# Optimization experiments

Hardware: AMD Instinct MI355X
Metric: run time of the kernel (lower is better)

The kernel has to match this reference:

```python
import jax, jax.numpy as jnp
import numpy as np
from jax import lax

EPS = 1e-8
ROOT_2 = 1.41421
STYLE_SIZE = 512
OUT_CH = 512
STYLE_SCALE = (2.0 / STYLE_SIZE) ** 0.5   # Weight_Scaling(style_size): equalized-LR sqrt(2/fan_in)
OUT_SCALE = (2.0 / (OUT_CH * 1 * 1)) ** 0.5  # Weight_Scaling(out_channels*1*1)


def setup_inputs() -> dict:
    key = jax.random.key(0)
    ks = jax.random.split(key, 10)
    B, Cin, Cout, H, S = 8, 512, 512, 32, 512
    return {
        "x": jax.random.normal(ks[0], (B, Cin, H, H), dtype=jnp.float32),
        "style_base": jax.random.normal(ks[1], (B, S), dtype=jnp.float32),
        "noise": jax.random.normal(ks[2], (B, 1, 2 * H, 2 * H), dtype=jnp.float32),
        "t": jax.random.normal(ks[3], (B, Cout, 2 * H, 2 * H), dtype=jnp.float32),
        # learned params
        "affine_w": jax.random.normal(ks[4], (Cin, S), dtype=jnp.float32) * (1.0 / np.sqrt(S)),
        "affine_b": jnp.zeros((Cin,), dtype=jnp.float32),
        "conv_w": jax.random.normal(ks[5], (Cout, Cin, 3, 3), dtype=jnp.float32),
        "conv_b": jnp.zeros((1, Cout, 1, 1), dtype=jnp.float32),
        "prelu_a": jnp.asarray(0.25, dtype=jnp.float32),
        "noise_scalar": jnp.zeros((1, Cout, 1, 1), dtype=jnp.float32) + 0.1,
        "out_w": jax.random.normal(ks[6], (3, Cout, 1, 1), dtype=jnp.float32) * (1.0 / np.sqrt(Cout)),
        "out_b": jnp.zeros((3,), dtype=jnp.float32),
    }


def reference(x, style_base, noise, t, affine_w, affine_b, conv_w, conv_b,
              prelu_a, noise_scalar, out_w, out_b):
    B, Cin, H, W = x.shape
    # style_std = affine(Weight_Scaling(style_base)) + 1  -> [B, Cin]
    style_std = (style_base * STYLE_SCALE) @ affine_w.T + affine_b + 1.0

    # bilinear x2 upsample (align_corners=False == half-pixel, matches jax.image.resize)
    x = jax.image.resize(x, (B, Cin, 2 * H, 2 * W), method="bilinear")

    # modulated conv with L2 demodulation, expressed as input-scale + conv + output-scale
    # per-sample weight w_b[o,i,k,l] = w[o,i,k,l]*s[b,i] / ||w*s||_b,o
    wsq = jnp.sum(conv_w ** 2, axis=(2, 3))                      # [O, I]
    demod = 1.0 / jnp.sqrt(jnp.einsum("oi,bi->bo", wsq, style_std ** 2) + EPS)  # [B, O]
    xm = x * style_std[:, :, None, None]
    y = lax.conv_general_dilated(xm, conv_w, (1, 1), "SAME",
                                 dimension_numbers=("NCHW", "OIHW", "NCHW"))
    y = y * demod[:, :, None, None] + conv_b + noise_scalar * noise
    # PReLU (single shared slope)
    y = jnp.where(y >= 0, y, prelu_a * y)

    # out branch: skip add, scale, toRGB 1x1 conv, clamp
    y = (y + t) / ROOT_2
    out = lax.conv_general_dilated(y * OUT_SCALE, out_w, (1, 1), "SAME",
                                   dimension_numbers=("NCHW", "OIHW", "NCHW"))
    out = jnp.clip(out + out_b[None, :, None, None], 0.0, 1.0)
    return (y, out)
```

## Files before the change

kernel.cpp:

```cpp
#include <hip/hip_runtime.h>


typedef short bf16x8 __attribute__((ext_vector_type(8)));
typedef short short8v __attribute__((ext_vector_type(8)));
typedef float f32x16 __attribute__((ext_vector_type(16)));

#define WS_STYLE 0
#define WS_DEMOD 16384
#define WS_WSQ   32768
#define WS_WPACK 1081344
#define WS_XM    5799936

__device__ __forceinline__ short f2bf(float f) {
  unsigned u = __float_as_uint(f);
  u += 0x7FFFu + ((u >> 16) & 1u);
  return (short)(u >> 16);
}

__device__ __forceinline__ void gld16(const short* g, char* l) {
  __builtin_amdgcn_global_load_lds((const __attribute__((address_space(1))) void*)g,
                                   (__attribute__((address_space(3))) void*)l,
                                   16, 0, 0);
}

__global__ void k_style(const float* __restrict__ sb, const float* __restrict__ aw,
                        const float* __restrict__ ab, float* __restrict__ style) {
  __shared__ float s_sb[512];
  int b = blockIdx.x;
  for (int i = threadIdx.x; i < 512; i += 256) s_sb[i] = sb[b * 512 + i] * 0.0625f;
  __syncthreads();
  for (int i = threadIdx.x; i < 512; i += 256) {
    const float4* wrow = (const float4*)(aw + (size_t)i * 512);
    float acc = 0.f;
    #pragma unroll 4
    for (int s4 = 0; s4 < 128; ++s4) {
      float4 w4 = wrow[s4];
      float4 sv = *(const float4*)(s_sb + s4 * 4);
      acc += w4.x * sv.x + w4.y * sv.y + w4.z * sv.z + w4.w * sv.w;
    }
    style[b * 512 + i] = acc + ab[i] + 1.0f;
  }
}

__global__ void k_wsq(const float* __restrict__ cw, float* __restrict__ wsq) {
  int idx = blockIdx.x * 256 + threadIdx.x;
  const float* p = cw + (size_t)idx * 9;
  float s = 0.f;
  #pragma unroll
  for (int j = 0; j < 9; ++j) s += p[j] * p[j];
  wsq[idx] = s;
}

__global__ void k_demod(const float* __restrict__ wsq, const float* __restrict__ style,
                        float* __restrict__ demod) {
  int wid = threadIdx.x >> 6, lane = threadIdx.x & 63;
  int idx = blockIdx.x * 4 + wid;
  int b = idx >> 9, o = idx & 511;
  const float* wr = wsq + (size_t)o * 512;
  const float* ss = style + b * 512;
  float sum = 0.f;
  #pragma unroll
  for (int k = 0; k < 8; ++k) {
    int i = k * 64 + lane;
    float s = ss[i];
    sum += wr[i] * s * s;
  }
  #pragma unroll
  for (int off = 32; off; off >>= 1) sum += __shfl_down(sum, off);
  if (lane == 0) demod[b * 512 + o] = rsqrtf(sum + 1e-8f);
}

__global__ void k_upsample(const float* __restrict__ x, const float* __restrict__ style,
                           short* __restrict__ xm) {
  int b = blockIdx.x / 66, hp = blockIdx.x % 66;
  short* xmp = xm + ((size_t)b * 66 + hp) * 66 * 512;
  if (hp == 0 || hp == 65) {
    short8v z = {0, 0, 0, 0, 0, 0, 0, 0};
    for (int u = threadIdx.x; u < 66 * 512 / 8; u += 256) ((short8v*)xmp)[u] = z;
    return;
  }
  int h = hp - 1;
  int j0 = (h >> 1) - 1 + (h & 1);
  float fj = (h & 1) ? 0.25f : 0.75f;
  int j0c = j0 < 0 ? 0 : j0;
  int j1c = j0 + 1 > 31 ? 31 : j0 + 1;
  __shared__ float xt[2][64][33];
  int ccc = threadIdx.x & 63;
  int wsub = threadIdx.x >> 6;
  for (int c0 = 0; c0 < 512; c0 += 64) {
    __syncthreads();
    #pragma unroll 4
    for (int k = 0; k < 16; ++k) {
      int idx = k * 256 + threadIdx.x;
      int ii = idx & 31, cc = (idx >> 5) & 63, jj = idx >> 11;
      xt[jj][cc][ii] = x[(((size_t)b * 512 + c0 + cc) * 32 + (jj ? j1c : j0c)) * 32 + ii];
    }
    __syncthreads();
    float sstyle = style[b * 512 + c0 + ccc];
    #pragma unroll 4
    for (int wk = 0; wk < 16; ++wk) {
      int w = wk * 4 + wsub;
      int i0 = (w >> 1) - 1 + (w & 1);
      float fi = (w & 1) ? 0.25f : 0.75f;
      int i0c = i0 < 0 ? 0 : i0;
      int i1c = i0 + 1 > 31 ? 31 : i0 + 1;
      float v0 = xt[0][ccc][i0c] * (1.f - fi) + xt[0][ccc][i1c] * fi;
      float v1 = xt[1][ccc][i0c] * (1.f - fi) + xt[1][ccc][i1c] * fi;
      float v = (v0 * (1.f - fj) + v1 * fj) * sstyle;
      xmp[(size_t)(w + 1) * 512 + c0 + ccc] = f2bf(v);
    }
    if (wsub == 0) {
      xmp[c0 + ccc] = 0;
      xmp[(size_t)65 * 512 + c0 + ccc] = 0;
    }
  }
}

__global__ void k_packw(const float* __restrict__ cw, short* __restrict__ wpk) {
  int unit = blockIdx.x * 256 + threadIdx.x;
  int s = unit >> 11;
  int rem = unit & 2047;
  int o = rem >> 2, kg = rem & 3;
  int tap = s >> 4, cc = s & 15;
  int i0 = cc * 32 + (kg << 3);
  const float* src = cw + ((size_t)o * 512 + i0) * 9 + tap;
  short8v v;
  #pragma unroll
  for (int j = 0; j < 8; ++j) v[j] = f2bf(src[j * 9]);
  *(short8v*)(wpk + (size_t)unit * 8) = v;
}

__global__ __launch_bounds__(256, 2) void k_conv(
    const short* __restrict__ xm, const short* __restrict__ wpk,
    const float* __restrict__ demod, const float* __restrict__ convb,
    const float* __restrict__ nscal, const float* __restrict__ noise,
    const float* __restrict__ t, const float* __restrict__ prelu_a,
    float* __restrict__ y) {
  __shared__ char XMs[2][16896];

  int tid = threadIdx.x;
  int bid = blockIdx.x;
  int nt = bid & 1, hpair = (bid >> 1) & 31, b = bid >> 6;
  int wid = tid >> 6, lane = tid & 63;
  int wo = wid & 1, wsrow = wid >> 1;
  int l31 = lane & 31, lg = lane >> 5;

  const short* xb = xm + ((size_t)b * 66 + hpair * 2) * 66 * 512;
  const short* wlp = wpk + (size_t)((nt * 256 + wo * 128 + l31) * 32 + lg * 8);

  #pragma unroll
  for (int k = 0; k < 4; ++k) {
    int u = k * 256 + tid;
    int r = u / 264, rem = u - r * 264;
    int wp = rem >> 2, spp = rem & 3;
    gld16(xb + (size_t)(r * 66 + wp) * 512 + ((spp ^ ((wp >> 1) & 3)) << 3), XMs[0] + u * 16);
  }
  if (tid < 32) {
    int u = 1024 + tid;
    int rem = u - 792;
    int wp = rem >> 2, spp = rem & 3;
    gld16(xb + (size_t)(3 * 66 + wp) * 512 + ((spp ^ ((wp >> 1) & 3)) << 3), XMs[0] + u * 16);
  }

  bf16x8 wc0 = *(const bf16x8*)(wlp + 0);
  bf16x8 wc1 = *(const bf16x8*)(wlp + 1024);
  bf16x8 wc2 = *(const bf16x8*)(wlp + 2048);
  bf16x8 wc3 = *(const bf16x8*)(wlp + 3072);
  bf16x8 wc4 = *(const bf16x8*)(wlp + 16);
  bf16x8 wc5 = *(const bf16x8*)(wlp + 1040);
  bf16x8 wc6 = *(const bf16x8*)(wlp + 2064);
  bf16x8 wc7 = *(const bf16x8*)(wlp + 3088);

  f32x16 zf = {0,0,0,0,0,0,0,0,0,0,0,0,0,0,0,0};
  f32x16 acc[4][2];
  #pragma unroll
  for (int i = 0; i < 4; ++i) { acc[i][0] = zf; acc[i][1] = zf; }

  asm volatile("s_waitcnt vmcnt(0) lgkmcnt(0)" ::: "memory");
  __builtin_amdgcn_s_barrier();
  __builtin_amdgcn_sched_barrier(0);

  #pragma unroll 1
  for (int cc = 0; cc < 16; ++cc) {
    const char* XMc = XMs[cc & 1];
    char* XMn = XMs[(cc & 1) ^ 1];
    #pragma unroll
    for (int tap = 0; tap < 9; ++tap) {
      const int kh = tap / 3, kw = tap % 3;

      bf16x8 wn0, wn1, wn2, wn3, wn4, wn5, wn6, wn7;
      {
        int ntap = (tap < 8) ? (tap + 1) : 0;
        int ncc  = (tap < 8) ? cc : (cc + 1 < 16 ? cc + 1 : 15);
        const short* wsrc = wlp + (size_t)(ntap * 16 + ncc) * 16384;
        wn0 = *(const bf16x8*)(wsrc + 0);
        wn1 = *(const bf16x8*)(wsrc + 1024);
        wn2 = *(const bf16x8*)(wsrc + 2048);
        wn3 = *(const bf16x8*)(wsrc + 3072);
        wn4 = *(const bf16x8*)(wsrc + 16);
        wn5 = *(const bf16x8*)(wsrc + 1040);
        wn6 = *(const bf16x8*)(wsrc + 2064);
        wn7 = *(const bf16x8*)(wsrc + 3088);
      }
      if (tap <= 5 && cc < 15 && tid < 176) {
        int u = tap * 176 + tid;
        int r = u / 264, rem = u - r * 264;
        int wp = rem >> 2, spp = rem & 3;
        gld16(xb + (size_t)(r * 66 + wp) * 512 + (cc + 1) * 32 + ((spp ^ ((wp >> 1) & 3)) << 3),
              XMn + u * 16);
      }

      int a = l31 + kw;
      int xo = ((wsrow + kh) * 66 + a) * 64 + ((lg ^ ((a >> 1) & 3)) << 4);
      bf16x8 xf00 = *(const bf16x8*)(XMc + xo);
      bf16x8 xf01 = *(const bf16x8*)(XMc + xo + 2048);
      bf16x8 xf10 = *(const bf16x8*)(XMc + (xo ^ 32));
      bf16x8 xf11 = *(const bf16x8*)(XMc + ((xo ^ 32) + 2048));

      __builtin_amdgcn_s_setprio(1);
      acc[0][0] = __builtin_amdgcn_mfma_f32_32x32x16_bf16(wc0, xf00, acc[0][0], 0, 0, 0);
      acc[0][1] = __builtin_amdgcn_mfma_f32_32x32x16_bf16(wc0, xf01, acc[0][1], 0, 0, 0);
      acc[1][0] = __builtin_amdgcn_mfma_f32_32x32x16_bf16(wc1, xf00, acc[1][0], 0, 0, 0);
      acc[1][1] = __builtin_amdgcn_mfma_f32_32x32x16_bf16(wc1, xf01, acc[1][1], 0, 0, 0);
      acc[2][0] = __builtin_amdgcn_mfma_f32_32x32x16_bf16(wc2, xf00, acc[2][0], 0, 0, 0);
      acc[2][1] = __builtin_amdgcn_mfma_f32_32x32x16_bf16(wc2, xf01, acc[2][1], 0, 0, 0);
      acc[3][0] = __builtin_amdgcn_mfma_f32_32x32x16_bf16(wc3, xf00, acc[3][0], 0, 0, 0);
      acc[3][1] = __builtin_amdgcn_mfma_f32_32x32x16_bf16(wc3, xf01, acc[3][1], 0, 0, 0);
      acc[0][0] = __builtin_amdgcn_mfma_f32_32x32x16_bf16(wc4, xf10, acc[0][0], 0, 0, 0);
      acc[0][1] = __builtin_amdgcn_mfma_f32_32x32x16_bf16(wc4, xf11, acc[0][1], 0, 0, 0);
      acc[1][0] = __builtin_amdgcn_mfma_f32_32x32x16_bf16(wc5, xf10, acc[1][0], 0, 0, 0);
      acc[1][1] = __builtin_amdgcn_mfma_f32_32x32x16_bf16(wc5, xf11, acc[1][1], 0, 0, 0);
      acc[2][0] = __builtin_amdgcn_mfma_f32_32x32x16_bf16(wc6, xf10, acc[2][0], 0, 0, 0);
      acc[2][1] = __builtin_amdgcn_mfma_f32_32x32x16_bf16(wc6, xf11, acc[2][1], 0, 0, 0);
      acc[3][0] = __builtin_amdgcn_mfma_f32_32x32x16_bf16(wc7, xf10, acc[3][0], 0, 0, 0);
      acc[3][1] = __builtin_amdgcn_mfma_f32_32x32x16_bf16(wc7, xf11, acc[3][1], 0, 0, 0);
      __builtin_amdgcn_s_setprio(0);

      wc0 = wn0; wc1 = wn1; wc2 = wn2; wc3 = wn3;
      wc4 = wn4; wc5 = wn5; wc6 = wn6; wc7 = wn7;

      if (tap == 8) {
        asm volatile("s_waitcnt vmcnt(0) lgkmcnt(0)" ::: "memory");
        __builtin_amdgcn_s_barrier();
        __builtin_amdgcn_sched_barrier(0);
      }
    }
  }

  float pa = prelu_a[0];
  const float inv_r2 = 1.0f / 1.41421f;
  int h = hpair * 2 + wsrow;
  float nz0 = noise[((size_t)b * 64 + h) * 64 + l31];
  float nz1 = noise[((size_t)b * 64 + h) * 64 + 32 + l31];
  #pragma unroll
  for (int cf = 0; cf < 4; ++cf) {
    #pragma unroll
    for (int reg = 0; reg < 16; ++reg) {
      int orow = (reg & 3) + 8 * (reg >> 2) + 4 * lg;
      int o = nt * 256 + wo * 128 + cf * 32 + orow;
      float dm = demod[b * 512 + o];
      float cb = convb[o];
      float ns = nscal[o];
      #pragma unroll
      for (int nf = 0; nf < 2; ++nf) {
        int w = nf * 32 + l31;
        float v = acc[cf][nf][reg];
        v = v * dm + cb + ns * (nf ? nz1 : nz0);
        v = (v >= 0.f) ? v : pa * v;
        size_t oi = (((size_t)b * 512 + o) * 64 + h) * 64 + w;
        v = (v + t[oi]) * inv_r2;
        y[oi] = v;
      }
    }
  }
}

__global__ void k_rgb(const float* __restrict__ y, const float* __restrict__ ow,
                      const float* __restrict__ ob, float* __restrict__ out) {
  int b = blockIdx.x >> 6, h = blockIdx.x & 63;
  int w = threadIdx.x & 63, g = threadIdx.x >> 6;
  const float* yb = y + (((size_t)b * 512) * 64 + h) * 64 + w;
  float s0 = 0.f, s1 = 0.f, s2 = 0.f;
  for (int o = g * 128; o < g * 128 + 128; ++o) {
    float v = yb[(size_t)o * 4096];
    s0 += v * ow[o];
    s1 += v * ow[512 + o];
    s2 += v * ow[1024 + o];
  }
  __shared__ float red[3][4][64];
  red[0][g][w] = s0; red[1][g][w] = s1; red[2][g][w] = s2;
  __syncthreads();
  if (threadIdx.x < 192) {
    int c = threadIdx.x >> 6, ww = threadIdx.x & 63;
    float s = red[c][0][ww] + red[c][1][ww] + red[c][2][ww] + red[c][3][ww];
    s = s * 0.0625f + ob[c];
    s = fminf(fmaxf(s, 0.f), 1.f);
    out[(((size_t)b * 3 + c) * 64 + h) * 64 + ww] = s;
  }
}

extern "C" void kernel_launch(void* const* d_in, const int* in_sizes, int n_in,
                              void* d_out, int out_size, void* d_ws, size_t ws_size,
                              hipStream_t stream) {
  const float* x     = (const float*)d_in[0];
  const float* sb    = (const float*)d_in[1];
  const float* noise = (const float*)d_in[2];
  const float* t     = (const float*)d_in[3];
  const float* aw    = (const float*)d_in[4];
  const float* ab    = (const float*)d_in[5];
  const float* cw    = (const float*)d_in[6];
  const float* cb    = (const float*)d_in[7];
  const float* pa    = (const float*)d_in[8];
  const float* ns    = (const float*)d_in[9];
  const float* ow    = (const float*)d_in[10];
  const float* ob    = (const float*)d_in[11];
  char* ws = (char*)d_ws;
  float* style = (float*)(ws + WS_STYLE);
  float* demod = (float*)(ws + WS_DEMOD);
  float* wsq   = (float*)(ws + WS_WSQ);
  short* wpk   = (short*)(ws + WS_WPACK);
  short* xm    = (short*)(ws + WS_XM);
  float* y   = (float*)d_out;
  float* out = y + 16777216;

  k_style<<<8, 256, 0, stream>>>(sb, aw, ab, style);
  k_wsq<<<1024, 256, 0, stream>>>(cw, wsq);
  k_demod<<<1024, 256, 0, stream>>>(wsq, style, demod);
  k_upsample<<<528, 256, 0, stream>>>(x, style, xm);
  k_packw<<<1152, 256, 0, stream>>>(cw, wpk);
  k_conv<<<512, 256, 0, stream>>>(xm, wpk, demod, cb, ns, noise, t, pa, y);
  k_rgb<<<512, 256, 0, stream>>>(y, ow, ob, out);
}
```

Measured before the change: 254.6 us.

## Split conv block into eight waves with two-deep weight prefetch

```diff
diff --git a/kernel.cpp b/kernel.cpp
--- a/kernel.cpp
+++ b/kernel.cpp
@@ -130,7 +130,7 @@
   *(short8v*)(wpk + (size_t)unit * 8) = v;
 }
 
-__global__ __launch_bounds__(256, 2) void k_conv(
+__global__ __launch_bounds__(512, 4) void k_conv(
     const short* __restrict__ xm, const short* __restrict__ wpk,
     const float* __restrict__ demod, const float* __restrict__ convb,
     const float* __restrict__ nscal, const float* __restrict__ noise,
@@ -142,39 +142,42 @@
   int bid = blockIdx.x;
   int nt = bid & 1, hpair = (bid >> 1) & 31, b = bid >> 6;
   int wid = tid >> 6, lane = tid & 63;
-  int wo = wid & 1, wsrow = wid >> 1;
+  int wo = wid & 3, wsrow = wid >> 2;
   int l31 = lane & 31, lg = lane >> 5;
 
   const short* xb = xm + ((size_t)b * 66 + hpair * 2) * 66 * 512;
-  const short* wlp = wpk + (size_t)((nt * 256 + wo * 128 + l31) * 32 + lg * 8);
-
-  #pragma unroll
-  for (int k = 0; k < 4; ++k) {
-    int u = k * 256 + tid;
+  const short* wlp = wpk + (size_t)((nt * 256 + wo * 64 + l31) * 32 + lg * 8);
+
+  {
+    int u = tid;
     int r = u / 264, rem = u - r * 264;
     int wp = rem >> 2, spp = rem & 3;
     gld16(xb + (size_t)(r * 66 + wp) * 512 + ((spp ^ ((wp >> 1) & 3)) << 3), XMs[0] + u * 16);
-  }
-  if (tid < 32) {
-    int u = 1024 + tid;
-    int rem = u - 792;
-    int wp = rem >> 2, spp = rem & 3;
-    gld16(xb + (size_t)(3 * 66 + wp) * 512 + ((spp ^ ((wp >> 1) & 3)) << 3), XMs[0] + u * 16);
-  }
-
-  bf16x8 wc0 = *(const bf16x8*)(wlp + 0);
-  bf16x8 wc1 = *(const bf16x8*)(wlp + 1024);
-  bf16x8 wc2 = *(const bf16x8*)(wlp + 2048);
-  bf16x8 wc3 = *(const bf16x8*)(wlp + 3072);
-  bf16x8 wc4 = *(const bf16x8*)(wlp + 16);
-  bf16x8 wc5 = *(const bf16x8*)(wlp + 1040);
-  bf16x8 wc6 = *(const bf16x8*)(wlp + 2064);
-  bf16x8 wc7 = *(const bf16x8*)(wlp + 3088);
+    u = 512 + tid;
+    r = u / 264; rem = u - r * 264;
+    wp = rem >> 2; spp = rem & 3;
+    gld16(xb + (size_t)(r * 66 + wp) * 512 + ((spp ^ ((wp >> 1) & 3)) << 3), XMs[0] + u * 16);
+    if (tid < 32) {
+      u = 1024 + tid;
+      rem = u - 792;
+      wp = rem >> 2; spp = rem & 3;
+      gld16(xb + (size_t)(3 * 66 + wp) * 512 + ((spp ^ ((wp >> 1) & 3)) << 3), XMs[0] + u * 16);
+    }
+  }
+
+  bf16x8 wcA = *(const bf16x8*)(wlp + 0);
+  bf16x8 wcC = *(const bf16x8*)(wlp + 16);
+  bf16x8 wcB = *(const bf16x8*)(wlp + 1024);
+  bf16x8 wcD = *(const bf16x8*)(wlp + 1040);
+  const short* w1p = wlp + 16 * 16384;
+  bf16x8 w1A = *(const bf16x8*)(w1p + 0);
+  bf16x8 w1C = *(const bf16x8*)(w1p + 16);
+  bf16x8 w1B = *(const bf16x8*)(w1p + 1024);
+  bf16x8 w1D = *(const bf16x8*)(w1p + 1040);
 
   f32x16 zf = {0,0,0,0,0,0,0,0,0,0,0,0,0,0,0,0};
-  f32x16 acc[4][2];
-  #pragma unroll
-  for (int i = 0; i < 4; ++i) { acc[i][0] = zf; acc[i][1] = zf; }
+  f32x16 acc[2][2];
+  acc[0][0] = zf; acc[0][1] = zf; acc[1][0] = zf; acc[1][1] = zf;
 
   asm volatile("s_waitcnt vmcnt(0) lgkmcnt(0)" ::: "memory");
   __builtin_amdgcn_s_barrier();
@@ -188,26 +191,37 @@
     for (int tap = 0; tap < 9; ++tap) {
       const int kh = tap / 3, kw = tap % 3;
 
-      bf16x8 wn0, wn1, wn2, wn3, wn4, wn5, wn6, wn7;
+      bf16x8 w2A, w2B, w2C, w2D;
       {
-        int ntap = (tap < 8) ? (tap + 1) : 0;
-        int ncc  = (tap < 8) ? cc : (cc + 1 < 16 ? cc + 1 : 15);
+        int ntap = (tap <= 6) ? (tap + 2) : (tap - 7);
+        int ncc  = (tap <= 6) ? cc : (cc + 1);
+        if (ncc > 15) ncc = 15;
         const short* wsrc = wlp + (size_t)(ntap * 16 + ncc) * 16384;
-        wn0 = *(const bf16x8*)(wsrc + 0);
-        wn1 = *(const bf16x8*)(wsrc + 1024);
-        wn2 = *(const bf16x8*)(wsrc + 2048);
-        wn3 = *(const bf16x8*)(wsrc + 3072);
-        wn4 = *(const bf16x8*)(wsrc + 16);
-        wn5 = *(const bf16x8*)(wsrc + 1040);
-        wn6 = *(const bf16x8*)(wsrc + 2064);
-        wn7 = *(const bf16x8*)(wsrc + 3088);
+        w2A = *(const bf16x8*)(wsrc + 0);
+        w2C = *(const bf16x8*)(wsrc + 16);
+        w2B = *(const bf16x8*)(wsrc + 1024);
+        w2D = *(const bf16x8*)(wsrc + 1040);
       }
-      if (tap <= 5 && cc < 15 && tid < 176) {
-        int u = tap * 176 + tid;
-        int r = u / 264, rem = u - r * 264;
-        int wp = rem >> 2, spp = rem & 3;
-        gld16(xb + (size_t)(r * 66 + wp) * 512 + (cc + 1) * 32 + ((spp ^ ((wp >> 1) & 3)) << 3),
-              XMn + u * 16);
+      if (cc < 15) {
+        if (tap == 0) {
+          int u = tid;
+          int r = u / 264, rem = u - r * 264;
+          int wp = rem >> 2, spp = rem & 3;
+          gld16(xb + (size_t)(r * 66 + wp) * 512 + (cc + 1) * 32 + ((spp ^ ((wp >> 1) & 3)) << 3),
+                XMn + u * 16);
+        } else if (tap == 1) {
+          int u = 512 + tid;
+          int r = u / 264, rem = u - r * 264;
+          int wp = rem >> 2, spp = rem & 3;
+          gld16(xb + (size_t)(r * 66 + wp) * 512 + (cc + 1) * 32 + ((spp ^ ((wp >> 1) & 3)) << 3),
+                XMn + u * 16);
+        } else if (tap == 2 && tid < 32) {
+          int u = 1024 + tid;
+          int rem = u - 792;
+          int wp = rem >> 2, spp = rem & 3;
+          gld16(xb + (size_t)(3 * 66 + wp) * 512 + (cc + 1) * 32 + ((spp ^ ((wp >> 1) & 3)) << 3),
+                XMn + u * 16);
+        }
       }
 
       int a = l31 + kw;
@@ -218,29 +232,22 @@
       bf16x8 xf11 = *(const bf16x8*)(XMc + ((xo ^ 32) + 2048));
 
       __builtin_amdgcn_s_setprio(1);
-      acc[0][0] = __builtin_amdgcn_mfma_f32_32x32x16_bf16(wc0, xf00, acc[0][0], 0, 0, 0);
-      acc[0][1] = __builtin_amdgcn_mfma_f32_32x32x16_bf16(wc0, xf01, acc[0][1], 0, 0, 0);
-      acc[1][0] = __builtin_amdgcn_mfma_f32_32x32x16_bf16(wc1, xf00, acc[1][0], 0, 0, 0);
-      acc[1][1] = __builtin_amdgcn_mfma_f32_32x32x16_bf16(wc1, xf01, acc[1][1], 0, 0, 0);
-      acc[2][0] = __builtin_amdgcn_mfma_f32_32x32x16_bf16(wc2, xf00, acc[2][0], 0, 0, 0);
-      acc[2][1] = __builtin_amdgcn_mfma_f32_32x32x16_bf16(wc2, xf01, acc[2][1], 0, 0, 0);
-      acc[3][0] = __builtin_amdgcn_mfma_f32_32x32x16_bf16(wc3, xf00, acc[3][0], 0, 0, 0);
-      acc[3][1] = __builtin_amdgcn_mfma_f32_32x32x16_bf16(wc3, xf01, acc[3][1], 0, 0, 0);
-      acc[0][0] = __builtin_amdgcn_mfma_f32_32x32x16_bf16(wc4, xf10, acc[0][0], 0, 0, 0);
-      acc[0][1] = __builtin_amdgcn_mfma_f32_32x32x16_bf16(wc4, xf11, acc[0][1], 0, 0, 0);
-      acc[1][0] = __builtin_amdgcn_mfma_f32_32x32x16_bf16(wc5, xf10, acc[1][0], 0, 0, 0);
-      acc[1][1] = __builtin_amdgcn_mfma_f32_32x32x16_bf16(wc5, xf11, acc[1][1], 0, 0, 0);
-      acc[2][0] = __builtin_amdgcn_mfma_f32_32x32x16_bf16(wc6, xf10, acc[2][0], 0, 0, 0);
-      acc[2][1] = __builtin_amdgcn_mfma_f32_32x32x16_bf16(wc6, xf11, acc[2][1], 0, 0, 0);
-      acc[3][0] = __builtin_amdgcn_mfma_f32_32x32x16_bf16(wc7, xf10, acc[3][0], 0, 0, 0);
-      acc[3][1] = __builtin_amdgcn_mfma_f32_32x32x16_bf16(wc7, xf11, acc[3][1], 0, 0, 0);
+      acc[0][0] = __builtin_amdgcn_mfma_f32_32x32x16_bf16(wcA, xf00, acc[0][0], 0, 0, 0);
+      acc[0][1] = __builtin_amdgcn_mfma_f32_32x32x16_bf16(wcA, xf01, acc[0][1], 0, 0, 0);
+      acc[1][0] = __builtin_amdgcn_mfma_f32_32x32x16_bf16(wcB, xf00, acc[1][0], 0, 0, 0);
+      acc[1][1] = __builtin_amdgcn_mfma_f32_32x32x16_bf16(wcB, xf01, acc[1][1], 0, 0, 0);
+      acc[0][0] = __builtin_amdgcn_mfma_f32_32x32x16_bf16(wcC, xf10, acc[0][0], 0, 0, 0);
+      acc[0][1] = __builtin_amdgcn_mfma_f32_32x32x16_bf16(wcC, xf11, acc[0][1], 0, 0, 0);
+      acc[1][0] = __builtin_amdgcn_mfma_f32_32x32x16_bf16(wcD, xf10, acc[1][0], 0, 0, 0);
+      acc[1][1] = __builtin_amdgcn_mfma_f32_32x32x16_bf16(wcD, xf11, acc[1][1], 0, 0, 0);
       __builtin_amdgcn_s_setprio(0);
 
-      wc0 = wn0; wc1 = wn1; wc2 = wn2; wc3 = wn3;
-      wc4 = wn4; wc5 = wn5; wc6 = wn6; wc7 = wn7;
+      wcA = w1A; wcB = w1B; wcC = w1C; wcD = w1D;
+      w1A = w2A; w1B = w2B; w1C = w2C; w1D = w2D;
 
       if (tap == 8) {
-        asm volatile("s_waitcnt vmcnt(0) lgkmcnt(0)" ::: "memory");
+        __builtin_amdgcn_sched_barrier(0);
+        asm volatile("s_waitcnt vmcnt(8) lgkmcnt(0)" ::: "memory");
         __builtin_amdgcn_s_barrier();
         __builtin_amdgcn_sched_barrier(0);
       }
@@ -253,19 +260,19 @@
   float nz0 = noise[((size_t)b * 64 + h) * 64 + l31];
   float nz1 = noise[((size_t)b * 64 + h) * 64 + 32 + l31];
   #pragma unroll
-  for (int cf = 0; cf < 4; ++cf) {
+  for (int cf = 0; cf < 2; ++cf) {
     #pragma unroll
     for (int reg = 0; reg < 16; ++reg) {
       int orow = (reg & 3) + 8 * (reg >> 2) + 4 * lg;
-      int o = nt * 256 + wo * 128 + cf * 32 + orow;
+      int o = nt * 256 + wo * 64 + cf * 32 + orow;
       float dm = demod[b * 512 + o];
       float cb = convb[o];
       float ns = nscal[o];
       #pragma unroll
-      for (int nf = 0; nf < 2; ++nf) {
-        int w = nf * 32 + l31;
-        float v = acc[cf][nf][reg];
-        v = v * dm + cb + ns * (nf ? nz1 : nz0);
+      for (int sf = 0; sf < 2; ++sf) {
+        int w = sf * 32 + l31;
+        float v = acc[cf][sf][reg];
+        v = v * dm + cb + ns * (sf ? nz1 : nz0);
         v = (v >= 0.f) ? v : pa * v;
         size_t oi = (((size_t)b * 512 + o) * 64 + h) * 64 + w;
         v = (v + t[oi]) * inv_r2;
@@ -328,6 +335,6 @@
   k_demod<<<1024, 256, 0, stream>>>(wsq, style, demod);
   k_upsample<<<528, 256, 0, stream>>>(x, style, xm);
   k_packw<<<1152, 256, 0, stream>>>(cw, wpk);
-  k_conv<<<512, 256, 0, stream>>>(xm, wpk, demod, cb, ns, noise, t, pa, y);
+  k_conv<<<512, 512, 0, stream>>>(xm, wpk, demod, cb, ns, noise, t, pa, y);
   k_rgb<<<512, 256, 0, stream>>>(y, ow, ob, out);
 }
```

Measured after the change: 716.6 us. 182% more time.
